# Kernel optimization log

Measured on AMD Instinct MI355X. Metric: run time of the kernel, lower is better.

## Reference

```python
import jax, jax.numpy as jnp
import numpy as np
import math

DIM = 128
HEADS = 8
HC = DIM // HEADS  # per-head channels = 16
N = 50000
E = 800000
LEAKY_SLOPE = 0.2


def _seg_softmax(logits, seg, n):
    # numerically-stable softmax over edges grouped by destination node
    m = jax.ops.segment_max(logits, seg, num_segments=n)
    m = jnp.where(jnp.isfinite(m), m, 0.0)
    e = jnp.exp(logits - m[seg])
    s = jax.ops.segment_sum(e, seg, num_segments=n)
    return e / jnp.maximum(s[seg], 1e-16)


def setup_inputs() -> dict:
    key = jax.random.key(0)
    ks = jax.random.split(key, 20)
    sc = 1.0 / math.sqrt(DIM)
    inp = {
        "x": jax.random.normal(ks[0], (N, DIM), jnp.float32),
        "edge_index": jax.random.randint(ks[1], (2, E), 0, N, jnp.int64),
        # GATConv params
        "gat_w": jax.random.normal(ks[2], (DIM, DIM), jnp.float32) * sc,
        "gat_att_src": jax.random.normal(ks[3], (HEADS, HC), jnp.float32) * sc,
        "gat_att_dst": jax.random.normal(ks[4], (HEADS, HC), jnp.float32) * sc,
        "gat_b": jnp.zeros((DIM,), jnp.float32),
        # SAGEConv params (lin_l has bias, lin_r has none; normalize=True)
        "sage_wl": jax.random.normal(ks[5], (DIM, DIM), jnp.float32) * sc,
        "sage_bl": jnp.zeros((DIM,), jnp.float32),
        "sage_wr": jax.random.normal(ks[6], (DIM, DIM), jnp.float32) * sc,
        # TransformerConv params (q/k/v + skip, heads concat -> DIM)
        "tr_wq": jax.random.normal(ks[7], (DIM, DIM), jnp.float32) * sc,
        "tr_bq": jnp.zeros((DIM,), jnp.float32),
        "tr_wk": jax.random.normal(ks[8], (DIM, DIM), jnp.float32) * sc,
        "tr_bk": jnp.zeros((DIM,), jnp.float32),
        "tr_wv": jax.random.normal(ks[9], (DIM, DIM), jnp.float32) * sc,
        "tr_bv": jnp.zeros((DIM,), jnp.float32),
        "tr_wskip": jax.random.normal(ks[10], (DIM, DIM), jnp.float32) * sc,
        "tr_bskip": jnp.zeros((DIM,), jnp.float32),
        # fusion + layernorm
        "fus_w": jax.random.normal(ks[11], (3 * DIM, DIM), jnp.float32) * (1.0 / math.sqrt(3 * DIM)),
        "fus_b": jnp.zeros((DIM,), jnp.float32),
        "ln_g": jnp.ones((DIM,), jnp.float32),
        "ln_b": jnp.zeros((DIM,), jnp.float32),
    }
    return inp


def reference(x, edge_index, gat_w, gat_att_src, gat_att_dst, gat_b,
              sage_wl, sage_bl, sage_wr,
              tr_wq, tr_bq, tr_wk, tr_bk, tr_wv, tr_bv, tr_wskip, tr_bskip,
              fus_w, fus_b, ln_g, ln_b):
    n = x.shape[0]
    src, dst = edge_index[0], edge_index[1]  # messages flow src -> dst

    # ---- GATConv (adds self-loops, per-dst softmax attention) ----
    loop = jnp.arange(n, dtype=src.dtype)
    s2 = jnp.concatenate([src, loop])
    d2 = jnp.concatenate([dst, loop])
    h = (x @ gat_w).reshape(n, HEADS, HC)            # [N,H,C]
    a_src = (h * gat_att_src).sum(-1)                # [N,H]
    a_dst = (h * gat_att_dst).sum(-1)
    logits = jax.nn.leaky_relu(a_src[s2] + a_dst[d2], LEAKY_SLOPE)  # [E+N,H]
    alpha = _seg_softmax(logits, d2, n)
    gat_out = jax.ops.segment_sum(alpha[:, :, None] * h[s2], d2,
                                  num_segments=n).reshape(n, DIM) + gat_b

    # ---- SAGEConv (mean aggregation + root weight, L2-normalized) ----
    ones = jnp.ones(src.shape, x.dtype)
    deg = jax.ops.segment_sum(ones, dst, num_segments=n)
    nbr = jax.ops.segment_sum(x[src], dst, num_segments=n) / jnp.maximum(deg, 1.0)[:, None]
    sage_out = nbr @ sage_wl + sage_bl + x @ sage_wr
    sage_out = sage_out / jnp.maximum(
        jnp.linalg.norm(sage_out, axis=-1, keepdims=True), 1e-12)

    # ---- TransformerConv (scaled dot-product attn per dst + skip) ----
    q = (x @ tr_wq + tr_bq).reshape(n, HEADS, HC)
    k = (x @ tr_wk + tr_bk).reshape(n, HEADS, HC)
    v = (x @ tr_wv + tr_bv).reshape(n, HEADS, HC)
    t_logits = (q[dst] * k[src]).sum(-1) / math.sqrt(HC)  # [E,H]
    t_alpha = _seg_softmax(t_logits, dst, n)               # dropout off (eval)
    tr_out = jax.ops.segment_sum(t_alpha[:, :, None] * v[src], dst,
                                 num_segments=n).reshape(n, DIM)
    tr_out = tr_out + x @ tr_wskip + tr_bskip

    # ---- fusion + layernorm ----
    concat = jnp.concatenate([gat_out, sage_out, tr_out], axis=-1)
    out = concat @ fus_w + fus_b
    mu = out.mean(-1, keepdims=True)
    var = ((out - mu) ** 2).mean(-1, keepdims=True)
    return (out - mu) / jnp.sqrt(var + 1e-5) * ln_g + ln_b
```

## Files before the change

kernel.cpp:

```cpp
#include <hip/hip_runtime.h>
#include <hip/hip_bf16.h>
#include <math.h>

#define DIM 128
#define HEADS 8

typedef short short8 __attribute__((ext_vector_type(8)));
typedef float f32x4 __attribute__((ext_vector_type(4)));

#define GLD_LDS16(g, l) \
  __builtin_amdgcn_global_load_lds((const __attribute__((address_space(1))) void*)(g), \
                                   (__attribute__((address_space(3))) void*)(l), 16, 0, 0)

__device__ __forceinline__ float bf2f(unsigned short u) {
  union { unsigned int i; float f; } c; c.i = ((unsigned int)u) << 16; return c.f;
}
__device__ __forceinline__ unsigned short f2bf(float f) {
  __hip_bfloat16 h = __float2bfloat16(f);
  union { __hip_bfloat16 h; unsigned short u; } c; c.h = h; return c.u;
}
__device__ __forceinline__ float u_lo(unsigned int u) {
  union { unsigned int i; float f; } c; c.i = u << 16; return c.f;
}
__device__ __forceinline__ float u_hi(unsigned int u) {
  union { unsigned int i; float f; } c; c.i = u & 0xffff0000u; return c.f;
}

__global__ void prep_w(const float* __restrict__ gw, const float* __restrict__ wq,
                       const float* __restrict__ wk, const float* __restrict__ wv,
                       const float* __restrict__ wsk,
                       const float* __restrict__ bq, const float* __restrict__ bk,
                       const float* __restrict__ bv, const float* __restrict__ bsk,
                       const float* __restrict__ atts, const float* __restrict__ attd,
                       const float* __restrict__ swl, const float* __restrict__ swr,
                       const float* __restrict__ fw,
                       unsigned short* __restrict__ Wcat_t, float* __restrict__ Bcat,
                       unsigned short* __restrict__ sage_t, unsigned short* __restrict__ fus_t) {
  int i = blockIdx.x * 256 + threadIdx.x;
  if (i < 98304) {
    int c = i >> 7, k = i & 127;
    int s = c >> 7, j = c & 127;
    float val;
    if (s <= 4) {
      const float* w = (s == 0) ? gw : (s == 1) ? wq : (s == 2) ? wk : (s == 3) ? wv : wsk;
      val = w[k * 128 + j];
    } else {
      if (j < 8) {
        float acc = 0.f;
#pragma unroll
        for (int t = 0; t < 16; ++t) acc += gw[k * 128 + j * 16 + t] * atts[j * 16 + t];
        val = acc;
      } else if (j < 16) {
        int h = j - 8;
        float acc = 0.f;
#pragma unroll
        for (int t = 0; t < 16; ++t) acc += gw[k * 128 + h * 16 + t] * attd[h * 16 + t];
        val = acc;
      } else {
        val = 0.f;
      }
    }
    Wcat_t[i] = f2bf(val);
  } else if (i < 131072) {
    int t = i - 98304;
    int j = t >> 8, k = t & 255;
    float v = (k < 128) ? swl[k * 128 + j] : swr[(k - 128) * 128 + j];
    sage_t[t] = f2bf(v);
  } else if (i < 180224) {
    int t = i - 131072;
    int j = t / 384, k = t - j * 384;
    fus_t[t] = f2bf(fw[k * 128 + j]);
  } else if (i < 180992) {
    int c = i - 180224;
    int s = c >> 7, j = c & 127;
    Bcat[c] = (s == 1) ? bq[j] : (s == 2) ? bk[j] : (s == 3) ? bv[j] : (s == 4) ? bsk[j] : 0.f;
  }
}

__global__ void convert_x(const float* __restrict__ x, unsigned short* __restrict__ AG, int n) {
  int i = blockIdx.x * 256 + threadIdx.x;
  if (i >= n * 32) return;
  int idx = i * 4;
  float4 v = *(const float4*)(x + idx);
  ushort4 u;
  u.x = f2bf(v.x); u.y = f2bf(v.y); u.z = f2bf(v.z); u.w = f2bf(v.w);
  *(ushort4*)(AG + (size_t)(idx >> 7) * 512 + 384 + (idx & 127)) = u;
}

template <int EPI>
__global__ __launch_bounds__(256) void gemm128(
    const __hip_bfloat16* __restrict__ A0, int lda0,
    const __hip_bfloat16* __restrict__ A1, int lda1,
    const __hip_bfloat16* __restrict__ Bt, int K,
    const float* __restrict__ bias,
    unsigned short* __restrict__ AGo, float* __restrict__ Pq, float* __restrict__ Psk,
    float* __restrict__ aSo, float* __restrict__ aDo,
    unsigned short* __restrict__ FUSo, float* __restrict__ outF,
    const float* __restrict__ lng, const float* __restrict__ lnb,
    int M) {
  __shared__ char Asb[128 * 64];
  __shared__ char Bsb[128 * 64];
  int tid = threadIdx.x;
  int l = tid & 63, w = tid >> 6;
  int row0 = blockIdx.x * 128, col0 = blockIdx.y * 128;
  f32x4 acc[2][8] = {};

  for (int kt = 0; kt < K; kt += 32) {
    const __hip_bfloat16* Ap;
    int lda, kof;
    if (A1 != nullptr && kt >= 128) { Ap = A1; lda = lda1; kof = kt - 128; }
    else { Ap = A0; lda = lda0; kof = kt; }
#pragma unroll
    for (int it = 0; it < 2; ++it) {
      int c = it * 256 + tid;
      int r = c >> 2, cp = c & 3;
      int gp = cp ^ (r & 3);
      int gr = row0 + r; if (gr >= M) gr = M - 1;
      GLD_LDS16((const char*)(Ap + (size_t)gr * lda + kof) + gp * 16, Asb + c * 16);
    }
#pragma unroll
    for (int it = 0; it < 2; ++it) {
      int c = it * 256 + tid;
      int r = c >> 2, cp = c & 3;
      int gp = cp ^ (r & 3);
      GLD_LDS16((const char*)(Bt + (size_t)(col0 + r) * K + kt) + gp * 16, Bsb + c * 16);
    }
    __syncthreads();
    int g = l >> 4, ri = l & 15;
    short8 af[2], bfr[8];
#pragma unroll
    for (int m = 0; m < 2; ++m) {
      int r = w * 32 + m * 16 + ri;
      af[m] = *(const short8*)(Asb + r * 64 + ((g ^ (r & 3)) * 16));
    }
#pragma unroll
    for (int c4 = 0; c4 < 8; ++c4) {
      int r = c4 * 16 + ri;
      bfr[c4] = *(const short8*)(Bsb + r * 64 + ((g ^ (r & 3)) * 16));
    }
#pragma unroll
    for (int m = 0; m < 2; ++m)
#pragma unroll
      for (int c4 = 0; c4 < 8; ++c4)
        acc[m][c4] = __builtin_amdgcn_mfma_f32_16x16x32_bf16(af[m], bfr[c4], acc[m][c4], 0, 0, 0);
    __syncthreads();
  }

  int g = l >> 4, ri = l & 15;
  float bias_r[8];
#pragma unroll
  for (int c4 = 0; c4 < 8; ++c4) bias_r[c4] = bias[col0 + c4 * 16 + ri];

  if (EPI == 0) {
    int y = col0 >> 7;
    if (y == 5) {
#pragma unroll
      for (int m = 0; m < 2; ++m) {
#pragma unroll
        for (int j = 0; j < 4; ++j) {
          int row = row0 + w * 32 + m * 16 + g * 4 + j;
          if (row >= M) continue;
          float v = acc[m][0][j];
          if (ri < 8) aSo[row * HEADS + ri] = v;
          else        aDo[row * HEADS + (ri - 8)] = v;
        }
      }
    } else {
#pragma unroll
      for (int m = 0; m < 2; ++m) {
#pragma unroll
        for (int j = 0; j < 4; ++j) {
          int row = row0 + w * 32 + m * 16 + g * 4 + j;
          if (row >= M) continue;
#pragma unroll
          for (int c4 = 0; c4 < 8; ++c4) {
            int c = c4 * 16 + ri;
            float v = acc[m][c4][j] + bias_r[c4];
            if (y == 0)      AGo[(size_t)row * 512 + c] = f2bf(v);
            else if (y == 1) Pq[(size_t)row * 128 + c] = v;
            else if (y == 2) AGo[(size_t)row * 512 + 128 + c] = f2bf(v);
            else if (y == 3) AGo[(size_t)row * 512 + 256 + c] = f2bf(v);
            else             Psk[(size_t)row * 128 + c] = v;
          }
        }
      }
    }
  } else {
#pragma unroll
    for (int m = 0; m < 2; ++m) {
#pragma unroll
      for (int j = 0; j < 4; ++j) {
        int row = row0 + w * 32 + m * 16 + g * 4 + j;
        bool ok = (row < M);
        float v[8];
        float s = 0.f;
#pragma unroll
        for (int c4 = 0; c4 < 8; ++c4) {
          v[c4] = acc[m][c4][j] + bias_r[c4];
          if (EPI == 1) s += v[c4] * v[c4];
          else          s += v[c4];
        }
        s += __shfl_xor(s, 1); s += __shfl_xor(s, 2);
        s += __shfl_xor(s, 4); s += __shfl_xor(s, 8);
        if (EPI == 1) {
          float inv = 1.f / fmaxf(sqrtf(s), 1e-12f);
          if (ok) {
#pragma unroll
            for (int c4 = 0; c4 < 8; ++c4)
              FUSo[(size_t)row * 384 + 128 + c4 * 16 + ri] = f2bf(v[c4] * inv);
          }
        } else {
          float mu = s * (1.f / 128.f);
          float ss = 0.f;
#pragma unroll
          for (int c4 = 0; c4 < 8; ++c4) { float d = v[c4] - mu; ss += d * d; }
          ss += __shfl_xor(ss, 1); ss += __shfl_xor(ss, 2);
          ss += __shfl_xor(ss, 4); ss += __shfl_xor(ss, 8);
          float rstd = 1.f / sqrtf(ss * (1.f / 128.f) + 1e-5f);
          if (ok) {
#pragma unroll
            for (int c4 = 0; c4 < 8; ++c4) {
              int c = c4 * 16 + ri;
              outF[(size_t)row * 128 + c] = (v[c4] - mu) * rstd * lng[c] + lnb[c];
            }
          }
        }
      }
    }
  }
}

__global__ void deg_hist(const int* __restrict__ ei, int* __restrict__ deg, int E) {
  int e = blockIdx.x * 256 + threadIdx.x;
  if (e < E) atomicAdd(&deg[ei[E + e]], 1);
}

__global__ void bsum_k(const int* __restrict__ deg, int* __restrict__ bsum, int n) {
  int blk = blockIdx.x, t = threadIdx.x;
  int base = blk * 1024 + t * 4;
  int s = 0;
  if (base + 3 < n) {
    int4 d = *(const int4*)(deg + base);
    s = d.x + d.y + d.z + d.w;
  } else {
#pragma unroll
    for (int j = 0; j < 4; ++j) { int i = base + j; if (i < n) s += deg[i]; }
  }
  int lane = t & 63, wid = t >> 6;
  int x = s;
#pragma unroll
  for (int d = 1; d < 64; d <<= 1) { int y = __shfl_up(x, d); if (lane >= d) x += y; }
  __shared__ int wsum[4];
  if (lane == 63) wsum[wid] = x;
  __syncthreads();
  if (t == 0) bsum[blk] = wsum[0] + wsum[1] + wsum[2] + wsum[3];
}

__global__ void bscan_k(const int* __restrict__ bsum, int* __restrict__ bpref,
                        int* __restrict__ total_out, int nb) {
  int lane = threadIdx.x;
  int carry = 0;
  for (int base = 0; base < nb; base += 64) {
    int i = base + lane;
    int v = (i < nb) ? bsum[i] : 0;
    int x = v;
#pragma unroll
    for (int d = 1; d < 64; d <<= 1) { int y = __shfl_up(x, d); if (lane >= d) x += y; }
    if (i < nb) bpref[i] = carry + x - v;
    carry += __shfl(x, 63);
  }
  if (lane == 0) total_out[0] = carry;
}

__global__ void offs_k(const int* __restrict__ deg, const int* __restrict__ bpref,
                       int* __restrict__ offs, int* __restrict__ cursor, int n) {
  int blk = blockIdx.x, t = threadIdx.x;
  int base = blk * 1024 + t * 4;
  int d0 = 0, d1 = 0, d2 = 0, d3 = 0;
  if (base + 3 < n) {
    int4 d = *(const int4*)(deg + base);
    d0 = d.x; d1 = d.y; d2 = d.z; d3 = d.w;
  } else {
    if (base + 0 < n) d0 = deg[base + 0];
    if (base + 1 < n) d1 = deg[base + 1];
    if (base + 2 < n) d2 = deg[base + 2];
    if (base + 3 < n) d3 = deg[base + 3];
  }
  int s = d0 + d1 + d2 + d3;
  int lane = t & 63, wid = t >> 6;
  int x = s;
#pragma unroll
  for (int d = 1; d < 64; d <<= 1) { int y = __shfl_up(x, d); if (lane >= d) x += y; }
  __shared__ int wsum[4];
  if (lane == 63) wsum[wid] = x;
  __syncthreads();
  int woff = 0;
  for (int ww = 0; ww < wid; ++ww) woff += wsum[ww];
  int excl = bpref[blk] + woff + x - s;
  int p0 = excl, p1 = excl + d0, p2 = p1 + d1, p3 = p2 + d2;
  if (base + 0 < n) { offs[base + 0] = p0; cursor[base + 0] = p0; }
  if (base + 1 < n) { offs[base + 1] = p1; cursor[base + 1] = p1; }
  if (base + 2 < n) { offs[base + 2] = p2; cursor[base + 2] = p2; }
  if (base + 3 < n) { offs[base + 3] = p3; cursor[base + 3] = p3; }
}

__global__ void scatter_k(const int* __restrict__ ei, int* __restrict__ cursor,
                          int* __restrict__ csrc, int E) {
  int e = blockIdx.x * 256 + threadIdx.x;
  if (e >= E) return;
  int src = ei[e], dst = ei[E + e];
  int pos = atomicAdd(&cursor[dst], 1);
  csrc[pos] = src;
}

__global__ __launch_bounds__(256) void aggregate(
    const unsigned short* __restrict__ AG, const float* __restrict__ Pq,
    const float* __restrict__ Psk,
    const float* __restrict__ aS, const float* __restrict__ aD,
    const int* __restrict__ offs, const int* __restrict__ csrc,
    const float* __restrict__ gat_b,
    unsigned short* __restrict__ FUS, unsigned short* __restrict__ nbrb, int n) {
  int node = blockIdx.x * 4 + (threadIdx.x >> 6);
  if (node >= n) return;
  int lane = threadIdx.x & 63;
  int head = lane >> 3;
  float2 qv = *(const float2*)(Pq + (size_t)node * 128 + 2 * lane);
  float adst = aD[node * HEADS + head];

  float lg0 = aS[node * HEADS + head] + adst;
  lg0 = fmaxf(lg0, 0.2f * lg0);
  float w0 = __expf(lg0);
  const char* Anb = (const char*)AG + ((size_t)node << 10) + lane * 4;
  unsigned int hu0 = *(const unsigned int*)(Anb);
  float2 acc_g = { w0 * u_lo(hu0), w0 * u_hi(hu0) };
  float l_g = w0;

  float l_t = 0.f;
  float2 acc_t = {0.f, 0.f};
  float2 acc_s = {0.f, 0.f};

  int e0 = offs[node], e1 = offs[node + 1];

#define EDGE_UPDATE(HU, KU, VU, XU, AV)                                  \
  {                                                                      \
    float lg = (AV) + adst;                                              \
    lg = fmaxf(lg, 0.2f * lg);                                           \
    float wg = __expf(lg);                                               \
    acc_g.x += wg * u_lo(HU);                                            \
    acc_g.y += wg * u_hi(HU);                                            \
    l_g += wg;                                                           \
    float part = qv.x * u_lo(KU) + qv.y * u_hi(KU);                      \
    part += __shfl_xor(part, 1);                                         \
    part += __shfl_xor(part, 2);                                         \
    part += __shfl_xor(part, 4);                                         \
    float wt = __expf(part * 0.25f);                                     \
    acc_t.x += wt * u_lo(VU);                                            \
    acc_t.y += wt * u_hi(VU);                                            \
    l_t += wt;                                                           \
    acc_s.x += u_lo(XU);                                                 \
    acc_s.y += u_hi(XU);                                                 \
  }

#define LOAD_EDGE(u, si_a, hu_a, ku_a, vu_a, xu_a, av_a)                 \
  {                                                                      \
    const char* As = (const char*)AG + ((size_t)si_a[u] << 10) + lane * 4; \
    hu_a[u] = *(const unsigned int*)(As);                                \
    ku_a[u] = *(const unsigned int*)(As + 256);                          \
    vu_a[u] = *(const unsigned int*)(As + 512);                          \
    xu_a[u] = *(const unsigned int*)(As + 768);                          \
    av_a[u] = aS[si_a[u] * HEADS + head];                                \
  }

  int e = e0;
  for (; e + 8 <= e1; e += 8) {
    int si[8];
#pragma unroll
    for (int u = 0; u < 8; ++u) si[u] = csrc[e + u];
    unsigned int hu[8], ku[8], vu[8], xu[8];
    float av[8];
#pragma unroll
    for (int u = 0; u < 8; ++u) LOAD_EDGE(u, si, hu, ku, vu, xu, av);
#pragma unroll
    for (int u = 0; u < 8; ++u) EDGE_UPDATE(hu[u], ku[u], vu[u], xu[u], av[u]);
  }
  if (e + 4 <= e1) {
    int si[4];
#pragma unroll
    for (int u = 0; u < 4; ++u) si[u] = csrc[e + u];
    unsigned int hu[4], ku[4], vu[4], xu[4];
    float av[4];
#pragma unroll
    for (int u = 0; u < 4; ++u) LOAD_EDGE(u, si, hu, ku, vu, xu, av);
#pragma unroll
    for (int u = 0; u < 4; ++u) EDGE_UPDATE(hu[u], ku[u], vu[u], xu[u], av[u]);
    e += 4;
  }
  for (; e < e1; ++e) {
    int s = csrc[e];
    const char* As = (const char*)AG + ((size_t)s << 10) + lane * 4;
    unsigned int hu = *(const unsigned int*)(As);
    unsigned int ku = *(const unsigned int*)(As + 256);
    unsigned int vu = *(const unsigned int*)(As + 512);
    unsigned int xu = *(const unsigned int*)(As + 768);
    float av = aS[s * HEADS + head];
    EDGE_UPDATE(hu, ku, vu, xu, av);
  }
#undef EDGE_UPDATE
#undef LOAD_EDGE

  float gx = acc_g.x / l_g + gat_b[2 * lane];
  float gy = acc_g.y / l_g + gat_b[2 * lane + 1];
  ushort2 go = { f2bf(gx), f2bf(gy) };
  *(ushort2*)(FUS + (size_t)node * 384 + 2 * lane) = go;

  float2 skip = *(const float2*)(Psk + (size_t)node * 128 + 2 * lane);
  float tx, ty;
  if (l_t > 0.f) {
    tx = acc_t.x / l_t + skip.x;
    ty = acc_t.y / l_t + skip.y;
  } else { tx = skip.x; ty = skip.y; }
  ushort2 to = { f2bf(tx), f2bf(ty) };
  *(ushort2*)(FUS + (size_t)node * 384 + 256 + 2 * lane) = to;

  float dg = fmaxf((float)(e1 - e0), 1.f);
  float inv = 1.f / dg;
  ushort2 nb = { f2bf(acc_s.x * inv), f2bf(acc_s.y * inv) };
  *(ushort2*)(nbrb + (size_t)node * 128 + 2 * lane) = nb;
}

extern "C" void kernel_launch(void* const* d_in, const int* in_sizes, int n_in,
                              void* d_out, int out_size, void* d_ws, size_t ws_size,
                              hipStream_t stream) {
  const float* x      = (const float*)d_in[0];
  const int*   ei     = (const int*)d_in[1];
  const float* gat_w  = (const float*)d_in[2];
  const float* att_s  = (const float*)d_in[3];
  const float* att_d  = (const float*)d_in[4];
  const float* gat_b  = (const float*)d_in[5];
  const float* swl    = (const float*)d_in[6];
  const float* sbl    = (const float*)d_in[7];
  const float* swr    = (const float*)d_in[8];
  const float* wq     = (const float*)d_in[9];
  const float* bq     = (const float*)d_in[10];
  const float* wk     = (const float*)d_in[11];
  const float* bk     = (const float*)d_in[12];
  const float* wv     = (const float*)d_in[13];
  const float* bv     = (const float*)d_in[14];
  const float* wsk    = (const float*)d_in[15];
  const float* bsk    = (const float*)d_in[16];
  const float* fus_w  = (const float*)d_in[17];
  const float* fus_b  = (const float*)d_in[18];
  const float* ln_g   = (const float*)d_in[19];
  const float* ln_b   = (const float*)d_in[20];
  float* out = (float*)d_out;

  const int n = in_sizes[0] / DIM;
  const int E = in_sizes[1] / 2;

  char* wsb = (char*)d_ws;
  size_t o = 0;
  auto carve = [&](size_t bytes) { char* p = wsb + o; o += (bytes + 255) & ~(size_t)255; return p; };
  unsigned short* Wcat_t = (unsigned short*)carve(768 * 128 * 2);
  float*          Bcat   = (float*)carve(768 * 4);
  unsigned short* sage_t = (unsigned short*)carve(128 * 256 * 2);
  unsigned short* fus_t  = (unsigned short*)carve(128 * 384 * 2);
  unsigned short* AG     = (unsigned short*)carve((size_t)n * 512 * 2);
  float*          Pqs    = (float*)carve((size_t)n * 128 * 4);
  float*          Psk    = (float*)carve((size_t)n * 128 * 4);
  float*          aS     = (float*)carve((size_t)n * HEADS * 4);
  float*          aD     = (float*)carve((size_t)n * HEADS * 4);
  unsigned short* FUS    = (unsigned short*)carve((size_t)n * 384 * 2);
  unsigned short* nbrb   = (unsigned short*)carve((size_t)n * 128 * 2);
  int* ideg   = (int*)carve((size_t)n * 4);
  int* offs   = (int*)carve(((size_t)n + 1) * 4);
  int* cursor = (int*)carve((size_t)n * 4);
  int* csrc   = (int*)carve((size_t)E * 4);
  const int NB = (n + 1023) / 1024;
  int* bsum   = (int*)carve((size_t)NB * 4);
  int* bpref  = (int*)carve((size_t)NB * 4);

  hipMemsetAsync(ideg, 0, n * sizeof(int), stream);

  prep_w<<<(180992 + 255) / 256, 256, 0, stream>>>(
      gat_w, wq, wk, wv, wsk, bq, bk, bv, bsk, att_s, att_d, swl, swr, fus_w,
      Wcat_t, Bcat, sage_t, fus_t);
  convert_x<<<(n * 32 + 255) / 256, 256, 0, stream>>>(x, AG, n);

  const int RB = (n + 127) / 128;

  gemm128<0><<<dim3(RB, 6), 256, 0, stream>>>(
      (const __hip_bfloat16*)(AG + 384), 512, nullptr, 0,
      (const __hip_bfloat16*)Wcat_t, 128, Bcat,
      AG, Pqs, Psk, aS, aD, nullptr, nullptr, nullptr, nullptr, n);

  deg_hist<<<(E + 255) / 256, 256, 0, stream>>>(ei, ideg, E);
  bsum_k<<<NB, 256, 0, stream>>>(ideg, bsum, n);
  bscan_k<<<1, 64, 0, stream>>>(bsum, bpref, offs + n, NB);
  offs_k<<<NB, 256, 0, stream>>>(ideg, bpref, offs, cursor, n);
  scatter_k<<<(E + 255) / 256, 256, 0, stream>>>(ei, cursor, csrc, E);

  aggregate<<<(n + 3) / 4, 256, 0, stream>>>(AG, Pqs, Psk, aS, aD, offs, csrc,
                                             gat_b, FUS, nbrb, n);

  gemm128<1><<<dim3(RB, 1), 256, 0, stream>>>(
      (const __hip_bfloat16*)nbrb, 128, (const __hip_bfloat16*)(AG + 384), 512,
      (const __hip_bfloat16*)sage_t, 256, sbl,
      nullptr, nullptr, nullptr, nullptr, nullptr,
      FUS, nullptr, nullptr, nullptr, n);

  gemm128<2><<<dim3(RB, 1), 256, 0, stream>>>(
      (const __hip_bfloat16*)FUS, 384, nullptr, 0,
      (const __hip_bfloat16*)fus_t, 384, fus_b,
      nullptr, nullptr, nullptr, nullptr, nullptr,
      nullptr, out, ln_g, ln_b, n);
}
```

Measured before the change: 419.2 us.

## Pack gathered node rows into mixed fp8/bf16 layout and fuse conversion with degree histogram

Shrinks the per-source gathered row from 1024 bytes to 672 bytes. K stays bf16, the GAT features and V become fp8 e4m3, x becomes e5m2, and the source attention logit moves into the same row, so each edge gather fetches fewer bytes in fewer separate requests. A separate bf16 copy of x is kept for the GEMMs. The x conversion and the degree histogram are merged into one launch so the histogram overlaps the conversion work. The cost is lower precision in the gathered GAT, V and neighbour-mean values, plus extra per-element fp8 decode ALU work.

```diff
diff --git a/kernel.cpp b/kernel.cpp
--- a/kernel.cpp
+++ b/kernel.cpp
@@ -1,9 +1,12 @@
 #include <hip/hip_runtime.h>
 #include <hip/hip_bf16.h>
+#include <hip/hip_fp16.h>
+#include <hip/hip_fp8.h>
 #include <math.h>
 
 #define DIM 128
 #define HEADS 8
+#define ROWB 672
 
 typedef short short8 __attribute__((ext_vector_type(8)));
 typedef float f32x4 __attribute__((ext_vector_type(4)));
@@ -24,6 +27,21 @@
 }
 __device__ __forceinline__ float u_hi(unsigned int u) {
   union { unsigned int i; float f; } c; c.i = u & 0xffff0000u; return c.f;
+}
+__device__ __forceinline__ unsigned char f_fp8(float f) {
+  __hip_fp8_e4m3 t(f);
+  return (unsigned char)t.__x;
+}
+__device__ __forceinline__ float fp8_f(unsigned char b) {
+  __hip_fp8_e4m3 t; t.__x = (__hip_fp8_storage_t)b; return (float)t;
+}
+__device__ __forceinline__ unsigned char f_e5m2(float f) {
+  unsigned short u = __half_as_ushort(__float2half(f));
+  unsigned short r = (unsigned short)((u + 0x7F + ((u >> 8) & 1)) >> 8);
+  return (unsigned char)r;
+}
+__device__ __forceinline__ float e5m2_f(unsigned char b) {
+  return __half2float(__ushort_as_half((unsigned short)(((unsigned short)b) << 8)));
 }
 
 __global__ void prep_w(const float* __restrict__ gw, const float* __restrict__ wq,
@@ -77,14 +95,25 @@
   }
 }
 
-__global__ void convert_x(const float* __restrict__ x, unsigned short* __restrict__ AG, int n) {
-  int i = blockIdx.x * 256 + threadIdx.x;
-  if (i >= n * 32) return;
-  int idx = i * 4;
-  float4 v = *(const float4*)(x + idx);
-  ushort4 u;
-  u.x = f2bf(v.x); u.y = f2bf(v.y); u.z = f2bf(v.z); u.w = f2bf(v.w);
-  *(ushort4*)(AG + (size_t)(idx >> 7) * 512 + 384 + (idx & 127)) = u;
+__global__ void conv_hist(const float* __restrict__ x, unsigned short* __restrict__ Xb,
+                          unsigned char* __restrict__ AG,
+                          const int* __restrict__ ei, int* __restrict__ ideg,
+                          int n, int E, int CB) {
+  int b = blockIdx.x;
+  if (b < CB) {
+    int i = b * 256 + threadIdx.x;
+    if (i >= n * 32) return;
+    int node = i >> 5, c = (i & 31) * 4;
+    float4 v = *(const float4*)(x + (size_t)node * 128 + c);
+    ushort4 ub = { f2bf(v.x), f2bf(v.y), f2bf(v.z), f2bf(v.w) };
+    *(ushort4*)(Xb + (size_t)node * 128 + c) = ub;
+    uchar4 u8 = { f_e5m2(v.x), f_e5m2(v.y), f_e5m2(v.z), f_e5m2(v.w) };
+    *(uchar4*)(AG + (size_t)node * ROWB + 512 + c) = u8;
+  } else {
+    int t = (b - CB) * 256 + threadIdx.x;
+    int stride = (gridDim.x - CB) * 256;
+    for (int e = t; e < E; e += stride) atomicAdd(&ideg[ei[E + e]], 1);
+  }
 }
 
 template <int EPI>
@@ -93,8 +122,8 @@
     const __hip_bfloat16* __restrict__ A1, int lda1,
     const __hip_bfloat16* __restrict__ Bt, int K,
     const float* __restrict__ bias,
-    unsigned short* __restrict__ AGo, float* __restrict__ Pq, float* __restrict__ Psk,
-    float* __restrict__ aSo, float* __restrict__ aDo,
+    unsigned char* __restrict__ AGo, float* __restrict__ Pq, float* __restrict__ Psk,
+    float* __restrict__ aDo,
     unsigned short* __restrict__ FUSo, float* __restrict__ outF,
     const float* __restrict__ lng, const float* __restrict__ lnb,
     int M) {
@@ -161,7 +190,7 @@
           int row = row0 + w * 32 + m * 16 + g * 4 + j;
           if (row >= M) continue;
           float v = acc[m][0][j];
-          if (ri < 8) aSo[row * HEADS + ri] = v;
+          if (ri < 8) *(float*)(AGo + (size_t)row * ROWB + 640 + ri * 4) = v;
           else        aDo[row * HEADS + (ri - 8)] = v;
         }
       }
@@ -176,10 +205,10 @@
           for (int c4 = 0; c4 < 8; ++c4) {
             int c = c4 * 16 + ri;
             float v = acc[m][c4][j] + bias_r[c4];
-            if (y == 0)      AGo[(size_t)row * 512 + c] = f2bf(v);
+            if (y == 0)      AGo[(size_t)row * ROWB + 256 + c] = f_fp8(v);
             else if (y == 1) Pq[(size_t)row * 128 + c] = v;
-            else if (y == 2) AGo[(size_t)row * 512 + 128 + c] = f2bf(v);
-            else if (y == 3) AGo[(size_t)row * 512 + 256 + c] = f2bf(v);
+            else if (y == 2) *(unsigned short*)(AGo + (size_t)row * ROWB + c * 2) = f2bf(v);
+            else if (y == 3) AGo[(size_t)row * ROWB + 384 + c] = f_fp8(v);
             else             Psk[(size_t)row * 128 + c] = v;
           }
         }
@@ -228,11 +257,6 @@
       }
     }
   }
-}
-
-__global__ void deg_hist(const int* __restrict__ ei, int* __restrict__ deg, int E) {
-  int e = blockIdx.x * 256 + threadIdx.x;
-  if (e < E) atomicAdd(&deg[ei[E + e]], 1);
 }
 
 __global__ void bsum_k(const int* __restrict__ deg, int* __restrict__ bsum, int n) {
@@ -314,9 +338,8 @@
 }
 
 __global__ __launch_bounds__(256) void aggregate(
-    const unsigned short* __restrict__ AG, const float* __restrict__ Pq,
-    const float* __restrict__ Psk,
-    const float* __restrict__ aS, const float* __restrict__ aD,
+    const unsigned char* __restrict__ AG, const float* __restrict__ Pq,
+    const float* __restrict__ Psk, const float* __restrict__ aD,
     const int* __restrict__ offs, const int* __restrict__ csrc,
     const float* __restrict__ gat_b,
     unsigned short* __restrict__ FUS, unsigned short* __restrict__ nbrb, int n) {
@@ -327,12 +350,13 @@
   float2 qv = *(const float2*)(Pq + (size_t)node * 128 + 2 * lane);
   float adst = aD[node * HEADS + head];
 
-  float lg0 = aS[node * HEADS + head] + adst;
+  const unsigned char* An = AG + (size_t)node * ROWB;
+  float lg0 = *(const float*)(An + 640 + head * 4) + adst;
   lg0 = fmaxf(lg0, 0.2f * lg0);
   float w0 = __expf(lg0);
-  const char* Anb = (const char*)AG + ((size_t)node << 10) + lane * 4;
-  unsigned int hu0 = *(const unsigned int*)(Anb);
-  float2 acc_g = { w0 * u_lo(hu0), w0 * u_hi(hu0) };
+  unsigned short h0raw = *(const unsigned short*)(An + 256 + lane * 2);
+  float2 acc_g = { w0 * fp8_f((unsigned char)(h0raw & 0xff)),
+                   w0 * fp8_f((unsigned char)(h0raw >> 8)) };
   float l_g = w0;
 
   float l_t = 0.f;
@@ -341,34 +365,34 @@
 
   int e0 = offs[node], e1 = offs[node + 1];
 
-#define EDGE_UPDATE(HU, KU, VU, XU, AV)                                  \
+#define EDGE_UPDATE(KU, HR, VR, XR, AV)                                  \
   {                                                                      \
     float lg = (AV) + adst;                                              \
     lg = fmaxf(lg, 0.2f * lg);                                           \
     float wg = __expf(lg);                                               \
-    acc_g.x += wg * u_lo(HU);                                            \
-    acc_g.y += wg * u_hi(HU);                                            \
+    acc_g.x += wg * fp8_f((unsigned char)((HR) & 0xff));                 \
+    acc_g.y += wg * fp8_f((unsigned char)((HR) >> 8));                   \
     l_g += wg;                                                           \
     float part = qv.x * u_lo(KU) + qv.y * u_hi(KU);                      \
     part += __shfl_xor(part, 1);                                         \
     part += __shfl_xor(part, 2);                                         \
     part += __shfl_xor(part, 4);                                         \
     float wt = __expf(part * 0.25f);                                     \
-    acc_t.x += wt * u_lo(VU);                                            \
-    acc_t.y += wt * u_hi(VU);                                            \
+    acc_t.x += wt * fp8_f((unsigned char)((VR) & 0xff));                 \
+    acc_t.y += wt * fp8_f((unsigned char)((VR) >> 8));                   \
     l_t += wt;                                                           \
-    acc_s.x += u_lo(XU);                                                 \
-    acc_s.y += u_hi(XU);                                                 \
-  }
-
-#define LOAD_EDGE(u, si_a, hu_a, ku_a, vu_a, xu_a, av_a)                 \
+    acc_s.x += e5m2_f((unsigned char)((XR) & 0xff));                     \
+    acc_s.y += e5m2_f((unsigned char)((XR) >> 8));                       \
+  }
+
+#define LOAD_EDGE(u, si_a, ku_a, hr_a, vr_a, xr_a, av_a)                 \
   {                                                                      \
-    const char* As = (const char*)AG + ((size_t)si_a[u] << 10) + lane * 4; \
-    hu_a[u] = *(const unsigned int*)(As);                                \
-    ku_a[u] = *(const unsigned int*)(As + 256);                          \
-    vu_a[u] = *(const unsigned int*)(As + 512);                          \
-    xu_a[u] = *(const unsigned int*)(As + 768);                          \
-    av_a[u] = aS[si_a[u] * HEADS + head];                                \
+    const unsigned char* As = AG + (size_t)si_a[u] * ROWB;               \
+    ku_a[u] = *(const unsigned int*)(As + lane * 4);                     \
+    hr_a[u] = *(const unsigned short*)(As + 256 + lane * 2);             \
+    vr_a[u] = *(const unsigned short*)(As + 384 + lane * 2);             \
+    xr_a[u] = *(const unsigned short*)(As + 512 + lane * 2);             \
+    av_a[u] = *(const float*)(As + 640 + head * 4);                      \
   }
 
   int e = e0;
@@ -376,34 +400,36 @@
     int si[8];
 #pragma unroll
     for (int u = 0; u < 8; ++u) si[u] = csrc[e + u];
-    unsigned int hu[8], ku[8], vu[8], xu[8];
+    unsigned int ku[8];
+    unsigned short hr[8], vr[8], xr[8];
     float av[8];
 #pragma unroll
-    for (int u = 0; u < 8; ++u) LOAD_EDGE(u, si, hu, ku, vu, xu, av);
-#pragma unroll
-    for (int u = 0; u < 8; ++u) EDGE_UPDATE(hu[u], ku[u], vu[u], xu[u], av[u]);
+    for (int u = 0; u < 8; ++u) LOAD_EDGE(u, si, ku, hr, vr, xr, av);
+#pragma unroll
+    for (int u = 0; u < 8; ++u) EDGE_UPDATE(ku[u], hr[u], vr[u], xr[u], av[u]);
   }
   if (e + 4 <= e1) {
     int si[4];
 #pragma unroll
     for (int u = 0; u < 4; ++u) si[u] = csrc[e + u];
-    unsigned int hu[4], ku[4], vu[4], xu[4];
+    unsigned int ku[4];
+    unsigned short hr[4], vr[4], xr[4];
     float av[4];
 #pragma unroll
-    for (int u = 0; u < 4; ++u) LOAD_EDGE(u, si, hu, ku, vu, xu, av);
-#pragma unroll
-    for (int u = 0; u < 4; ++u) EDGE_UPDATE(hu[u], ku[u], vu[u], xu[u], av[u]);
+    for (int u = 0; u < 4; ++u) LOAD_EDGE(u, si, ku, hr, vr, xr, av);
+#pragma unroll
+    for (int u = 0; u < 4; ++u) EDGE_UPDATE(ku[u], hr[u], vr[u], xr[u], av[u]);
     e += 4;
   }
   for (; e < e1; ++e) {
     int s = csrc[e];
-    const char* As = (const char*)AG + ((size_t)s << 10) + lane * 4;
-    unsigned int hu = *(const unsigned int*)(As);
-    unsigned int ku = *(const unsigned int*)(As + 256);
-    unsigned int vu = *(const unsigned int*)(As + 512);
-    unsigned int xu = *(const unsigned int*)(As + 768);
-    float av = aS[s * HEADS + head];
-    EDGE_UPDATE(hu, ku, vu, xu, av);
+    const unsigned char* As = AG + (size_t)s * ROWB;
+    unsigned int ku = *(const unsigned int*)(As + lane * 4);
+    unsigned short hr = *(const unsigned short*)(As + 256 + lane * 2);
+    unsigned short vr = *(const unsigned short*)(As + 384 + lane * 2);
+    unsigned short xr = *(const unsigned short*)(As + 512 + lane * 2);
+    float av = *(const float*)(As + 640 + head * 4);
+    EDGE_UPDATE(ku, hr, vr, xr, av);
   }
 #undef EDGE_UPDATE
 #undef LOAD_EDGE
@@ -464,11 +490,11 @@
   float*          Bcat   = (float*)carve(768 * 4);
   unsigned short* sage_t = (unsigned short*)carve(128 * 256 * 2);
   unsigned short* fus_t  = (unsigned short*)carve(128 * 384 * 2);
-  unsigned short* AG     = (unsigned short*)carve((size_t)n * 512 * 2);
+  unsigned char*  AG     = (unsigned char*)carve((size_t)n * ROWB);
+  unsigned short* Xb     = (unsigned short*)carve((size_t)n * 128 * 2);
   float*          Pqs    = (float*)carve((size_t)n * 128 * 4);
   float*          Psk    = (float*)carve((size_t)n * 128 * 4);
-  float*          aS     = (float*)carve((size_t)n * HEADS * 4);
-  float*          aD     = (float*)carve((size_t)n * HEADS * 4);
+  float*          aDa    = (float*)carve((size_t)n * HEADS * 4);
   unsigned short* FUS    = (unsigned short*)carve((size_t)n * 384 * 2);
   unsigned short* nbrb   = (unsigned short*)carve((size_t)n * 128 * 2);
   int* ideg   = (int*)carve((size_t)n * 4);
@@ -484,33 +510,35 @@
   prep_w<<<(180992 + 255) / 256, 256, 0, stream>>>(
       gat_w, wq, wk, wv, wsk, bq, bk, bv, bsk, att_s, att_d, swl, swr, fus_w,
       Wcat_t, Bcat, sage_t, fus_t);
-  convert_x<<<(n * 32 + 255) / 256, 256, 0, stream>>>(x, AG, n);
+
+  const int CB = (n * 32 + 255) / 256;
+  const int HB = (E + 255) / 256 / 2;
+  conv_hist<<<CB + HB, 256, 0, stream>>>(x, Xb, AG, ei, ideg, n, E, CB);
 
   const int RB = (n + 127) / 128;
 
   gemm128<0><<<dim3(RB, 6), 256, 0, stream>>>(
-      (const __hip_bfloat16*)(AG + 384), 512, nullptr, 0,
+      (const __hip_bfloat16*)Xb, 128, nullptr, 0,
       (const __hip_bfloat16*)Wcat_t, 128, Bcat,
-      AG, Pqs, Psk, aS, aD, nullptr, nullptr, nullptr, nullptr, n);
-
-  deg_hist<<<(E + 255) / 256, 256, 0, stream>>>(ei, ideg, E);
+      AG, Pqs, Psk, aDa, nullptr, nullptr, nullptr, nullptr, n);
+
   bsum_k<<<NB, 256, 0, stream>>>(ideg, bsum, n);
   bscan_k<<<1, 64, 0, stream>>>(bsum, bpref, offs + n, NB);
   offs_k<<<NB, 256, 0, stream>>>(ideg, bpref, offs, cursor, n);
   scatter_k<<<(E + 255) / 256, 256, 0, stream>>>(ei, cursor, csrc, E);
 
-  aggregate<<<(n + 3) / 4, 256, 0, stream>>>(AG, Pqs, Psk, aS, aD, offs, csrc,
+  aggregate<<<(n + 3) / 4, 256, 0, stream>>>(AG, Pqs, Psk, aDa, offs, csrc,
                                              gat_b, FUS, nbrb, n);
 
   gemm128<1><<<dim3(RB, 1), 256, 0, stream>>>(
-      (const __hip_bfloat16*)nbrb, 128, (const __hip_bfloat16*)(AG + 384), 512,
+      (const __hip_bfloat16*)nbrb, 128, (const __hip_bfloat16*)Xb, 128,
       (const __hip_bfloat16*)sage_t, 256, sbl,
-      nullptr, nullptr, nullptr, nullptr, nullptr,
+      nullptr, nullptr, nullptr, nullptr,
       FUS, nullptr, nullptr, nullptr, n);
 
   gemm128<2><<<dim3(RB, 1), 256, 0, stream>>>(
       (const __hip_bfloat16*)FUS, 384, nullptr, 0,
       (const __hip_bfloat16*)fus_t, 384, fus_b,
-      nullptr, nullptr, nullptr, nullptr, nullptr,
+      nullptr, nullptr, nullptr, nullptr,
       nullptr, out, ln_g, ln_b, n);
 }
```

Measured after the change: 379.2 us. 1.11x faster.
